# Kernel tuning notes

Hardware: AMD Instinct MI355X
Metric: run time of the kernel (lower is better)

## Reference

```python
import jax, jax.numpy as jnp
import numpy as np

L = 7  # window size (odd)
A = 0.1
B_COEF = 0.9


def mex_hat(d):
    grid = (np.mgrid[:d, :d] - d // 2) * 1.0
    eucl = (grid ** 2).sum(0) ** 0.5
    eucl /= d
    return eucl * np.exp(-eucl)


def setup_inputs() -> dict:
    key = jax.random.key(0)
    x = jax.random.normal(key, (16, 1, 512, 512), dtype=jnp.float32)
    kernel = jnp.asarray(mex_hat(L).reshape(-1), dtype=jnp.float32)  # [49], row-major like unfold
    return {"x": x, "kernel": kernel}


def reference(x, kernel):
    # x: [B,1,H,W], kernel: [L*L]
    # Extract zero-padded LxL patches, matching F.unfold(padding=L//2) ordering
    # (C=1, kernel positions row-major). patches: [B, L*L, H, W]
    patches = jax.lax.conv_general_dilated_patches(
        x, (L, L), (1, 1), 'SAME')
    average_term = jnp.exp(-patches.mean(axis=1, keepdims=True))  # [B,1,H,W]
    differential_term = jnp.sum(
        kernel[None, :, None, None] * jax.nn.relu(patches - x),
        axis=1, keepdims=True)  # [B,1,H,W]
    suppression = A * average_term + B_COEF * differential_term
    norm = jnp.sqrt(jnp.sum(suppression ** 2))
    suppression = suppression / norm
    mask = jnp.where(x > suppression, jnp.ones_like(x), jnp.zeros_like(x))
    return mask, average_term, differential_term
```

## Files before the change

### kernel.cpp

```cpp
#include <hip/hip_runtime.h>
#include <math.h>

#define HW 512
#define NB 16
#define TX 64
#define TY 64
#define LDSW 72
#define LDSH 70
#define N_PIX (NB * HW * HW)
#define NBLK (8 * 8 * NB)

using f32x4 = __attribute__((ext_vector_type(4))) float;

__device__ __forceinline__ float sgpr_f(float v) {
    return __uint_as_float(__builtin_amdgcn_readfirstlane(__float_as_uint(v)));
}

__global__ __launch_bounds__(256, 2) void li_phase1(
    const float* __restrict__ x, const float* __restrict__ kw,
    float* __restrict__ out_ratio, float* __restrict__ out_avg,
    float* __restrict__ out_dif, float* __restrict__ partials)
{
    __shared__ float tile[LDSH * LDSW];
    __shared__ float wsum[4];

    const int tid = threadIdx.x;
    const int bx = blockIdx.x, by = blockIdx.y, b = blockIdx.z;
    const int x0 = bx * TX, y0 = by * TY;
    const float* xb = x + (size_t)b * (HW * HW);

    float w[49];
    float W = 0.f;
#pragma unroll
    for (int i = 0; i < 49; i++) { w[i] = sgpr_f(kw[i]); W += w[i]; }

    for (int idx = tid; idx < LDSH * (LDSW / 4); idx += 256) {
        int r = idx / (LDSW / 4);
        int c4 = idx - r * (LDSW / 4);
        int gy = y0 - 3 + r;
        int gx = x0 - 4 + c4 * 4;
        float4 v = make_float4(0.f, 0.f, 0.f, 0.f);
        if ((unsigned)gy < HW && (unsigned)gx < HW)
            v = *(const float4*)(xb + gy * HW + gx);
        *(float4*)&tile[r * LDSW + c4 * 4] = v;
    }
    __syncthreads();

    const int cx = tid & 15;
    const int cy = tid >> 4;
    const int colw = 4 * cx;
    const int row0 = 4 * cy;

    float cen[16];
#pragma unroll
    for (int p = 0; p < 4; p++) {
        float4 c4v = *(const float4*)&tile[(row0 + 3 + p) * LDSW + colw + 4];
        cen[p*4+0] = c4v.x; cen[p*4+1] = c4v.y; cen[p*4+2] = c4v.z; cen[p*4+3] = c4v.w;
    }

    float dif[16], bsum[16];
#pragma unroll
    for (int k = 0; k < 16; k++) { dif[k] = 0.f; bsum[k] = 0.f; }

#pragma unroll
    for (int r = 0; r < 10; r++) {
        const float* base = &tile[(row0 + r) * LDSW + colw];
        float4 q0 = *(const float4*)base;
        float4 q1 = *(const float4*)(base + 4);
        float4 q2 = *(const float4*)(base + 8);
        float v[12] = {q0.x, q0.y, q0.z, q0.w,
                       q1.x, q1.y, q1.z, q1.w,
                       q2.x, q2.y, q2.z, q2.w};

        float s0 = ((v[1] + v[2]) + (v[3] + v[4])) + ((v[5] + v[6]) + v[7]);
        float s1 = s0 + (v[8]  - v[1]);
        float s2 = s1 + (v[9]  - v[2]);
        float s3 = s2 + (v[10] - v[3]);

#pragma unroll
        for (int p = 0; p < 4; p++) {
            const int di = r - p;
            if (di < 0 || di >= 7) continue;
            bsum[p*4+0] += s0; bsum[p*4+1] += s1;
            bsum[p*4+2] += s2; bsum[p*4+3] += s3;
#pragma unroll
            for (int dj = 0; dj < 7; dj++) {
                if (di == 3 && dj == 3) continue;
                const float wv = w[di*7+dj];
#pragma unroll
                for (int j = 0; j < 4; j++)
                    dif[p*4+j] = fmaf(wv, fmaxf(v[1+j+dj], cen[p*4+j]), dif[p*4+j]);
            }
        }
    }

    const size_t gbase = (size_t)b * (HW * HW) + (size_t)(y0 + row0) * HW + x0 + colw;
    float ss = 0.f;
#pragma unroll
    for (int p = 0; p < 4; p++) {
        float av[4], dv[4], rv[4];
#pragma unroll
        for (int j = 0; j < 4; j++) {
            const int k = p*4+j;
            av[j] = __expf(-bsum[k] * (1.0f / 49.0f));
            dv[j] = fmaf(-W, cen[k], dif[k]);
            const float spv = 0.1f * av[j] + 0.9f * dv[j];
            rv[j] = cen[k] * __builtin_amdgcn_rcpf(spv);
            ss = fmaf(spv, spv, ss);
        }
        const size_t gi = gbase + (size_t)p * HW;
        *(f32x4*)(out_avg + gi)   = (f32x4){av[0], av[1], av[2], av[3]};
        *(f32x4*)(out_dif + gi)   = (f32x4){dv[0], dv[1], dv[2], dv[3]};
        *(f32x4*)(out_ratio + gi) = (f32x4){rv[0], rv[1], rv[2], rv[3]};
    }

#pragma unroll
    for (int off = 32; off > 0; off >>= 1)
        ss += __shfl_down(ss, off, 64);
    if ((tid & 63) == 0) wsum[tid >> 6] = ss;
    __syncthreads();
    if (tid == 0)
        partials[bx + 8 * (by + 8 * b)] = (wsum[0] + wsum[1]) + (wsum[2] + wsum[3]);
}

__global__ __launch_bounds__(256) void li_phase2(
    const float* __restrict__ partials, float* __restrict__ io)
{
    __shared__ float wsum[4];
    __shared__ float s_inv;
    const int tid = threadIdx.x;

    float s = 0.f;
#pragma unroll
    for (int i = 0; i < NBLK / 256; i++)
        s += partials[tid + i * 256];
#pragma unroll
    for (int off = 32; off > 0; off >>= 1)
        s += __shfl_down(s, off, 64);
    if ((tid & 63) == 0) wsum[tid >> 6] = s;
    __syncthreads();
    if (tid == 0)
        s_inv = 1.0f / sqrtf((wsum[0] + wsum[1]) + (wsum[2] + wsum[3]));
    __syncthreads();

    const float inv = s_inv;
    const int base = blockIdx.x * 4096 + tid * 4;
#pragma unroll
    for (int k = 0; k < 4; k++) {
        const int i = base + k * 1024;
        float4 r = *(const float4*)(io + i);
        float4 m;
        m.x = (r.x > inv) ? 1.f : 0.f;
        m.y = (r.y > inv) ? 1.f : 0.f;
        m.z = (r.z > inv) ? 1.f : 0.f;
        m.w = (r.w > inv) ? 1.f : 0.f;
        *(float4*)(io + i) = m;
    }
}

extern "C" void kernel_launch(void* const* d_in, const int* in_sizes, int n_in,
                              void* d_out, int out_size, void* d_ws, size_t ws_size,
                              hipStream_t stream) {
    const float* x  = (const float*)d_in[0];
    const float* kw = (const float*)d_in[1];
    float* out   = (float*)d_out;
    float* ratio = out;
    float* avg   = out + N_PIX;
    float* dif   = out + 2 * (size_t)N_PIX;
    float* ws    = (float*)d_ws;

    dim3 g(HW / TX, HW / TY, NB);
    li_phase1<<<g, 256, 0, stream>>>(x, kw, ratio, avg, dif, ws);
    li_phase2<<<N_PIX / 4096, 256, 0, stream>>>(ws, ratio);
}
```

Measured before the change: 100.6 us.

## Replace LDS tile staging with direct global float4 loads and edge-specialized path

Removes the shared-memory halo tile and its barrier. Each thread now reads its 10 rows of 12 floats straight from global memory, relying on L1/L2 to absorb the overlap between neighbouring threads. A templated EDGE variant adds bounds checks only for border tiles. This saves LDS traffic and the sync, but raises global/cache load traffic about 7.5x per thread, and the per-row zero-fill of 4-float chunks at the image border depends on x0 being aligned to 4.

```diff
diff --git a/kernel.cpp b/kernel.cpp
--- a/kernel.cpp
+++ b/kernel.cpp
@@ -5,8 +5,6 @@
 #define NB 16
 #define TX 64
 #define TY 64
-#define LDSW 72
-#define LDSH 70
 #define N_PIX (NB * HW * HW)
 #define NBLK (8 * 8 * NB)
 
@@ -16,58 +14,45 @@
     return __uint_as_float(__builtin_amdgcn_readfirstlane(__float_as_uint(v)));
 }
 
-__global__ __launch_bounds__(256, 2) void li_phase1(
-    const float* __restrict__ x, const float* __restrict__ kw,
-    float* __restrict__ out_ratio, float* __restrict__ out_avg,
-    float* __restrict__ out_dif, float* __restrict__ partials)
+__device__ __forceinline__ float4 ld4g(const float* rowp, int c0, bool vrow) {
+    if (vrow && (unsigned)c0 <= (unsigned)(HW - 4))
+        return *(const float4*)(rowp + c0);
+    return make_float4(0.f, 0.f, 0.f, 0.f);
+}
+
+template<bool EDGE>
+__device__ __forceinline__ void tile_compute(
+    const float* __restrict__ xb, const float* __restrict__ w,
+    int x0, int y0, int colw, int row0,
+    float* __restrict__ cen, float* __restrict__ dif, float* __restrict__ bsum)
 {
-    __shared__ float tile[LDSH * LDSW];
-    __shared__ float wsum[4];
+    const int c0 = x0 + colw - 4;
 
-    const int tid = threadIdx.x;
-    const int bx = blockIdx.x, by = blockIdx.y, b = blockIdx.z;
-    const int x0 = bx * TX, y0 = by * TY;
-    const float* xb = x + (size_t)b * (HW * HW);
-
-    float w[49];
-    float W = 0.f;
-#pragma unroll
-    for (int i = 0; i < 49; i++) { w[i] = sgpr_f(kw[i]); W += w[i]; }
-
-    for (int idx = tid; idx < LDSH * (LDSW / 4); idx += 256) {
-        int r = idx / (LDSW / 4);
-        int c4 = idx - r * (LDSW / 4);
-        int gy = y0 - 3 + r;
-        int gx = x0 - 4 + c4 * 4;
-        float4 v = make_float4(0.f, 0.f, 0.f, 0.f);
-        if ((unsigned)gy < HW && (unsigned)gx < HW)
-            v = *(const float4*)(xb + gy * HW + gx);
-        *(float4*)&tile[r * LDSW + c4 * 4] = v;
-    }
-    __syncthreads();
-
-    const int cx = tid & 15;
-    const int cy = tid >> 4;
-    const int colw = 4 * cx;
-    const int row0 = 4 * cy;
-
-    float cen[16];
 #pragma unroll
     for (int p = 0; p < 4; p++) {
-        float4 c4v = *(const float4*)&tile[(row0 + 3 + p) * LDSW + colw + 4];
-        cen[p*4+0] = c4v.x; cen[p*4+1] = c4v.y; cen[p*4+2] = c4v.z; cen[p*4+3] = c4v.w;
+        const float* rowp = xb + (y0 + row0 + p) * HW;
+        float4 c4 = *(const float4*)(rowp + c0 + 4);
+        cen[p*4+0] = c4.x; cen[p*4+1] = c4.y; cen[p*4+2] = c4.z; cen[p*4+3] = c4.w;
     }
 
-    float dif[16], bsum[16];
 #pragma unroll
     for (int k = 0; k < 16; k++) { dif[k] = 0.f; bsum[k] = 0.f; }
 
 #pragma unroll
     for (int r = 0; r < 10; r++) {
-        const float* base = &tile[(row0 + r) * LDSW + colw];
-        float4 q0 = *(const float4*)base;
-        float4 q1 = *(const float4*)(base + 4);
-        float4 q2 = *(const float4*)(base + 8);
+        const int gy = y0 + row0 + r - 3;
+        const float* rowp = xb + gy * HW;
+        float4 q0, q1, q2;
+        if (EDGE) {
+            const bool vrow = (unsigned)gy < (unsigned)HW;
+            q0 = ld4g(rowp, c0,     vrow);
+            q1 = ld4g(rowp, c0 + 4, vrow);
+            q2 = ld4g(rowp, c0 + 8, vrow);
+        } else {
+            q0 = *(const float4*)(rowp + c0);
+            q1 = *(const float4*)(rowp + c0 + 4);
+            q2 = *(const float4*)(rowp + c0 + 8);
+        }
         float v[12] = {q0.x, q0.y, q0.z, q0.w,
                        q1.x, q1.y, q1.z, q1.w,
                        q2.x, q2.y, q2.z, q2.w};
@@ -93,6 +78,36 @@
             }
         }
     }
+}
+
+__global__ __launch_bounds__(256, 2) void li_phase1(
+    const float* __restrict__ x, const float* __restrict__ kw,
+    float* __restrict__ out_ratio, float* __restrict__ out_avg,
+    float* __restrict__ out_dif, float* __restrict__ partials)
+{
+    __shared__ float wsum[4];
+
+    const int tid = threadIdx.x;
+    const int bx = blockIdx.x, by = blockIdx.y, b = blockIdx.z;
+    const int x0 = bx * TX, y0 = by * TY;
+    const float* xb = x + (size_t)b * (HW * HW);
+
+    float w[49];
+    float W = 0.f;
+#pragma unroll
+    for (int i = 0; i < 49; i++) { w[i] = sgpr_f(kw[i]); W += w[i]; }
+
+    const int cx = tid & 15;
+    const int cy = tid >> 4;
+    const int colw = 4 * cx;
+    const int row0 = 4 * cy;
+
+    float cen[16], dif[16], bsum[16];
+    const bool edge = (bx == 0) | (bx == 7) | (by == 0) | (by == 7);
+    if (edge)
+        tile_compute<true >(xb, w, x0, y0, colw, row0, cen, dif, bsum);
+    else
+        tile_compute<false>(xb, w, x0, y0, colw, row0, cen, dif, bsum);
 
     const size_t gbase = (size_t)b * (HW * HW) + (size_t)(y0 + row0) * HW + x0 + colw;
     float ss = 0.f;
```

Result: no change. 100.8 us (+0.2%).
